# Performance work log

Hardware: AMD Instinct MI355X
Metric: run time of the kernel (lower is better)

The kernel has to match this reference:

```python
import jax, jax.numpy as jnp
import numpy as np

WL_W = 8   # wl_weight
WL_IN = 8  # wl_activate (input quantization)
EPS = 1e-5

def _wq(x, bits):
    # WAGE-style uniform quantize-dequantize to `bits` bits in [-1+step, 1-step], STE passthrough
    step = 2.0 ** (1 - bits)
    q = jnp.clip(jnp.round(x / step) * step, -1.0 + step, 1.0 - step)
    return x + jax.lax.stop_gradient(q - x)

def _qconv(x, w, b, pad):
    y = jax.lax.conv_general_dilated(
        _wq(x, WL_IN), _wq(w, WL_W), (1, 1), [(pad, pad), (pad, pad)],
        dimension_numbers=('NCHW', 'OIHW', 'NCHW'))
    return y + b[None, :, None, None]

def _bn_relu(x, g, be):
    # BatchNorm2d in training mode: batch statistics over (N, H, W)
    m = jnp.mean(x, axis=(0, 2, 3), keepdims=True)
    v = jnp.var(x, axis=(0, 2, 3), keepdims=True)
    return jax.nn.relu((x - m) * jax.lax.rsqrt(v + EPS) * g[None, :, None, None] + be[None, :, None, None])

def _maxpool3(x):
    # MaxPool2d(3, stride=1, padding=1)
    return jax.lax.reduce_window(x, -jnp.inf, jax.lax.max,
                                 (1, 1, 3, 3), (1, 1, 1, 1),
                                 [(0, 0), (0, 0), (1, 1), (1, 1)])

def setup_inputs() -> dict:
    key = jax.random.key(0)
    ks = jax.random.split(key, 8)
    d = {'x': jax.random.normal(ks[0], (128, 192, 32, 32), jnp.float32)}
    specs = [('b1', 1, 64, 192, 1), ('b2a', 2, 96, 192, 1), ('b2b', 3, 128, 96, 3),
             ('b3a', 4, 16, 192, 1), ('b3b', 5, 32, 16, 3), ('b3c', 6, 32, 32, 3),
             ('b4', 7, 32, 192, 1)]
    for name, i, co, ci, k in specs:
        d[name + '_w'] = jax.random.normal(ks[i], (co, ci, k, k), jnp.float32) * 0.05
        d[name + '_b'] = jnp.zeros((co,), jnp.float32)
        d[name + '_g'] = jnp.ones((co,), jnp.float32)
        d[name + '_be'] = jnp.zeros((co,), jnp.float32)
    return d

def reference(x,
              b1_w, b1_b, b1_g, b1_be,
              b2a_w, b2a_b, b2a_g, b2a_be,
              b2b_w, b2b_b, b2b_g, b2b_be,
              b3a_w, b3a_b, b3a_g, b3a_be,
              b3b_w, b3b_b, b3b_g, b3b_be,
              b3c_w, b3c_b, b3c_g, b3c_be,
              b4_w, b4_b, b4_g, b4_be):
    y1 = _bn_relu(_qconv(x, b1_w, b1_b, 0), b1_g, b1_be)
    y2 = _bn_relu(_qconv(x, b2a_w, b2a_b, 0), b2a_g, b2a_be)
    y2 = _bn_relu(_qconv(y2, b2b_w, b2b_b, 1), b2b_g, b2b_be)
    y3 = _bn_relu(_qconv(x, b3a_w, b3a_b, 0), b3a_g, b3a_be)
    y3 = _bn_relu(_qconv(y3, b3b_w, b3b_b, 1), b3b_g, b3b_be)
    y3 = _bn_relu(_qconv(y3, b3c_w, b3c_b, 1), b3c_g, b3c_be)
    y4 = _bn_relu(_qconv(_maxpool3(x), b4_w, b4_b, 0), b4_g, b4_be)
    return jnp.concatenate([y1, y2, y3, y4], axis=1)  # [N, 256, 32, 32]
```

## Files before the change

### kernel.cpp

```cpp
#include <hip/hip_runtime.h>

typedef unsigned short u16;
typedef unsigned int u32;
typedef __attribute__((ext_vector_type(4))) int i32x4;
typedef __attribute__((ext_vector_type(4))) float f32x4;
typedef __attribute__((ext_vector_type(4))) u16 u16x4;
typedef __attribute__((ext_vector_type(8))) u16 u16x8;

#define PTOT 131072
#define NREP 16

static __device__ __forceinline__ int qi8(float v) {
  int q = (int)rintf(v * 128.f);
  return max(-127, min(127, q));
}
static __device__ __forceinline__ u16 bf_rne(float v) {
  u32 u = __float_as_uint(v);
  u += 0x7fffu + ((u >> 16) & 1u);
  return (u16)(u >> 16);
}
static __device__ __forceinline__ float bf2f(u16 v) {
  return __uint_as_float((u32)v << 16);
}

struct WPtrs { const float* p[7]; };

__global__ void wpack_kernel(WPtrs wp, char* __restrict__ o) {
  static const int S[7][5] = {
      {0,      192, 192, 1, 64},
      {12288,  192, 192, 1, 96},
      {30720,  96,  320, 3, 128},
      {153600, 192, 192, 1, 16},
      {156672, 16,  64,  3, 32},
      {162816, 32,  128, 3, 32},
      {175104, 192, 192, 1, 32},
  };
  int idx = blockIdx.x * 256 + threadIdx.x;
  if (idx >= 181248) return;
  int s = 0;
#pragma unroll
  for (int i = 1; i < 7; ++i)
    if (idx >= S[i][0]) s = i;
  int local = idx - S[s][0];
  int CIr = S[s][1], KROWP = S[s][2], KH = S[s][3], Co = S[s][4];
  int j = local & 15, lane = (local >> 4) & 63, f = local >> 10;
  int NF = Co >> 4;
  int c = f / NF, nf = f - c * NF;
  int co = nf * 16 + (lane & 15);
  int k = c * 64 + ((lane >> 4) << 4) + j;
  int r = k / KROWP, kk = k - r * KROWP;
  char val = 0;
  if (kk < 3 * CIr || KH == 1) {
    int kw = (KH == 1) ? 0 : (kk / CIr);
    int ci = (KH == 1) ? kk : (kk - kw * CIr);
    val = (char)qi8(wp.p[s][(((size_t)co * CIr + ci) * KH + r) * KH + kw]);
  }
  o[idx] = val;
}

__global__ __launch_bounds__(256) void quantx_kernel(const float* __restrict__ x,
                                                     char* __restrict__ xq) {
  __shared__ __align__(16) char tile[64][80];
  int n = blockIdx.z, hwb = blockIdx.x * 64, cb = blockIdx.y * 64;
  int lane = threadIdx.x & 63, sub = threadIdx.x >> 6;
#pragma unroll
  for (int i = 0; i < 16; ++i) {
    int c = sub + i * 4;
    float v = x[(((size_t)n * 192 + cb + c) << 10) + hwb + lane];
    tile[lane][c] = (char)qi8(v);
  }
  __syncthreads();
  int t = threadIdx.x, px = t >> 2, c16 = t & 3;
  uint4 v = *(const uint4*)&tile[px][c16 * 16];
  *(uint4*)&xq[(((size_t)n << 10) + hwb + px) * 192 + cb + c16 * 16] = v;
}

__global__ __launch_bounds__(256) void pool_kernel(const char* __restrict__ xq,
                                                   char* __restrict__ xpq) {
  int idx = blockIdx.x * 256 + threadIdx.x;
  int c16 = idx % 12;
  int p = idx / 12;
  int n = p >> 10, hw = p & 1023, h = hw >> 5, w = hw & 31;
  int m[16];
#pragma unroll
  for (int j = 0; j < 16; ++j) m[j] = -127;
  for (int dh = -1; dh <= 1; ++dh) {
    int hh = h + dh; if (hh < 0 || hh > 31) continue;
    for (int dw = -1; dw <= 1; ++dw) {
      int ww = w + dw; if (ww < 0 || ww > 31) continue;
      uint4 v = *(const uint4*)&xq[((((size_t)n << 5) + hh) * 32 + ww) * 192 + c16 * 16];
      const char* bb = reinterpret_cast<const char*>(&v);
#pragma unroll
      for (int t = 0; t < 16; ++t) {
        int b = (int)bb[t];
        m[t] = b > m[t] ? b : m[t];
      }
    }
  }
  uint4 o;
  char* ob = reinterpret_cast<char*>(&o);
#pragma unroll
  for (int t = 0; t < 16; ++t) ob[t] = (char)m[t];
  *(uint4*)&xpq[(size_t)p * 192 + c16 * 16] = o;
}

__global__ __launch_bounds__(256) void border_kernel(char* __restrict__ q2a,
                                                     char* __restrict__ q3a,
                                                     char* __restrict__ q3b) {
  int img = blockIdx.x, buf = blockIdx.y;
  char* base; int C;
  if (buf == 0) { base = q2a; C = 96; }
  else if (buf == 1) { base = q3a; C = 16; }
  else { base = q3b; C = 32; }
  char* ib = base + (size_t)img * 34 * 34 * C;
  int nch = C >> 4;
  uint4 z = {0, 0, 0, 0};
  for (int idx = threadIdx.x; idx < 132 * nch; idx += 256) {
    int b = idx / nch, cc = idx - b * nch;
    int h, w;
    if (b < 34) { h = 0; w = b; }
    else if (b < 68) { h = 33; w = b - 34; }
    else { int s = b - 68; h = 1 + (s >> 1); w = (s & 1) ? 33 : 0; }
    *(uint4*)(ib + ((h * 34 + w) * C + cc * 16)) = z;
  }
}

template <int NFW, int MF>
static __device__ __forceinline__ void conv_epilogue(
    i32x4 (&acc)[MF][NFW], int nfw, int lane, int wave, int mbase,
    u16* __restrict__ yh, double* __restrict__ stb, int ststride) {
  float yv[MF][NFW][4];
#pragma unroll
  for (int mf = 0; mf < MF; ++mf)
#pragma unroll
    for (int nf = 0; nf < NFW; ++nf)
      if (nf < nfw) {
        int col = nf * 16 + (lane & 15);
        int pix = mbase + mf * 16 + ((lane >> 4) << 2);
        u16x4 o;
#pragma unroll
        for (int r = 0; r < 4; ++r) {
          float v = (float)acc[mf][nf][r] * 6.103515625e-05f;
          yv[mf][nf][r] = v;
          o[r] = bf_rne(v);
        }
        *(u16x4*)&yh[(size_t)col * PTOT + pix] = o;
      }

  float s1[NFW], s2[NFW];
#pragma unroll
  for (int nf = 0; nf < NFW; ++nf) { s1[nf] = 0.f; s2[nf] = 0.f; }
#pragma unroll
  for (int mf = 0; mf < MF; ++mf)
#pragma unroll
    for (int nf = 0; nf < NFW; ++nf)
      if (nf < nfw)
#pragma unroll
        for (int r = 0; r < 4; ++r) {
          float v = yv[mf][nf][r];
          s1[nf] += v;
          s2[nf] += v * v;
        }
#pragma unroll
  for (int m = 16; m <= 32; m <<= 1)
#pragma unroll
    for (int nf = 0; nf < NFW; ++nf) {
      s1[nf] += __shfl_xor(s1[nf], m);
      s2[nf] += __shfl_xor(s2[nf], m);
    }
  __shared__ float red[4][NFW][16][2];
  if (lane < 16)
#pragma unroll
    for (int nf = 0; nf < NFW; ++nf) {
      red[wave][nf][lane][0] = s1[nf];
      red[wave][nf][lane][1] = s2[nf];
    }
  __syncthreads();
  const int t = threadIdx.x;
  if (t < 16 * nfw) {
    int nf = t >> 4, l = t & 15;
    float a = red[0][nf][l][0] + red[1][nf][l][0] + red[2][nf][l][0] + red[3][nf][l][0];
    float b = red[0][nf][l][1] + red[1][nf][l][1] + red[2][nf][l][1] + red[3][nf][l][1];
    int rep = blockIdx.x & (NREP - 1);
    atomicAdd(&stb[rep * ststride + 2 * t], (double)a);
    atomicAdd(&stb[rep * ststride + 2 * t + 1], (double)b);
  }
}

__global__ __launch_bounds__(256, 4) void cstat1x1_kernel(
    const char* __restrict__ xq, const char* __restrict__ xpq,
    const char* __restrict__ bpk, double* __restrict__ st, u16* __restrict__ yh) {
  constexpr int NFW = 6;
  constexpr int MF = 2;
  const int b = blockIdx.y;
  const int nfw = (b == 0) ? 4 : (b == 1) ? 6 : (b == 2) ? 1 : 2;
  const int bpo = (b == 0) ? 0 : (b == 1) ? 12288 : (b == 2) ? 153600 : 175104;
  const int sto = (b == 0) ? 0 : (b == 1) ? 256 * NREP
                           : (b == 2) ? 3 * 256 * NREP : 6 * 256 * NREP;
  const int yho = (b == 0) ? 0 : (b == 1) ? 64 : (b == 2) ? 160 : 176;
  const char* xin = (b == 3) ? xpq : xq;
  const char* bp = bpk + bpo;
  double* stb = st + sto;
  u16* yhb = yh + (size_t)yho * PTOT;

  const int lane = threadIdx.x & 63;
  const int wave = threadIdx.x >> 6;
  const int mbase = blockIdx.x * 128 + wave * 32;

  uint abase[MF];
#pragma unroll
  for (int mf = 0; mf < MF; ++mf)
    abase[mf] = (uint)(mbase + mf * 16 + (lane & 15)) * 192u;
  const uint klane = (uint)(lane >> 4) * 16u;
  const uint blane = (uint)lane * 16u;

  i32x4 acc[MF][NFW];
#pragma unroll
  for (int i = 0; i < MF; ++i)
#pragma unroll
    for (int j = 0; j < NFW; ++j) acc[i][j] = {0, 0, 0, 0};

#pragma unroll
  for (int c = 0; c < 3; ++c) {
    i32x4 af[MF];
#pragma unroll
    for (int mf = 0; mf < MF; ++mf)
      af[mf] = *(const i32x4*)(xin + (abase[mf] + (uint)c * 64u + klane));
    i32x4 bfr[NFW];
#pragma unroll
    for (int nf = 0; nf < NFW; ++nf)
      if (nf < nfw)
        bfr[nf] = *(const i32x4*)(bp + ((uint)((c * nfw + nf) * 1024) + blane));
#pragma unroll
    for (int mf = 0; mf < MF; ++mf)
#pragma unroll
      for (int nf = 0; nf < NFW; ++nf)
        if (nf < nfw)
          acc[mf][nf] = __builtin_amdgcn_mfma_i32_16x16x64_i8(af[mf], bfr[nf],
                                                              acc[mf][nf], 0, 0, 0);
  }

  conv_epilogue<NFW, MF>(acc, nfw, lane, wave, mbase, yhb, stb, 256);
}

template <int CI, int KROWP, int COB, int WPEU>
__global__ __launch_bounds__(256, WPEU) void cstat9_kernel(
    const char* __restrict__ xin, const char* __restrict__ bp, int nft,
    double* __restrict__ stb, u16* __restrict__ yh) {
  constexpr int CPR = KROWP / 64;
  constexpr int NCH = 3 * CPR;
  constexpr int NFW = COB / 16;
  constexpr int MF = 2;
  constexpr int TILE = 6 * 34 * CI;
  constexpr int TV = TILE / 16;

  __shared__ __align__(16) char atile[TILE + 64];

  const int lane = threadIdx.x & 63;
  const int wave = threadIdx.x >> 6;
  const int mbase = blockIdx.x * 128 + wave * 32;

  {
    int p0 = blockIdx.x * 128;
    int n = p0 >> 10, h0 = (p0 & 1023) >> 5;
    const char* src = xin + (size_t)((n * 34 + h0) * 34) * CI;
    for (int s = threadIdx.x; s < TV; s += 256)
      *(uint4*)&atile[s * 16] = *(const uint4*)(src + (size_t)s * 16);
  }
  __syncthreads();

  uint albase[MF];
#pragma unroll
  for (int mf = 0; mf < MF; ++mf) {
    int lp = wave * 32 + mf * 16 + (lane & 15);
    albase[mf] = (uint)(((lp >> 5) * 34 + (lp & 31)) * CI);
  }
  const uint klane = (uint)(lane >> 4) * 16u;
  const uint blane = (uint)lane * 16u;

  i32x4 acc[MF][NFW];
#pragma unroll
  for (int i = 0; i < MF; ++i)
#pragma unroll
    for (int j = 0; j < NFW; ++j) acc[i][j] = {0, 0, 0, 0};

#pragma unroll 2
  for (int c = 0; c < NCH; ++c) {
    int rr = c / CPR, o = (c - rr * CPR) * 64;
    uint koff = (uint)(rr * 34 * CI + o);
    i32x4 af[MF];
#pragma unroll
    for (int mf = 0; mf < MF; ++mf)
      af[mf] = *(const i32x4*)&atile[albase[mf] + koff + klane];
    i32x4 bfr[NFW];
#pragma unroll
    for (int nf = 0; nf < NFW; ++nf)
      bfr[nf] = *(const i32x4*)(bp + ((uint)((c * nft + nf) * 1024) + blane));
#pragma unroll
    for (int mf = 0; mf < MF; ++mf)
#pragma unroll
      for (int nf = 0; nf < NFW; ++nf)
        acc[mf][nf] = __builtin_amdgcn_mfma_i32_16x16x64_i8(af[mf], bfr[nf],
                                                            acc[mf][nf], 0, 0, 0);
  }

  conv_epilogue<NFW, MF>(acc, NFW, lane, wave, mbase, yh, stb, 256);
}

struct BnPtrs { const float* g[4]; const float* be[4]; };

__global__ __launch_bounds__(256) void bnout_all_kernel(
    const u16* __restrict__ yh, const double* __restrict__ st, BnPtrs bp,
    float* __restrict__ out) {
  int co = blockIdx.y, chunk = blockIdx.x, tid = threadIdx.x;
  int br = (co < 64) ? 0 : (co < 192) ? 1 : (co < 224) ? 2 : 3;
  int lco = co - ((br == 0) ? 0 : (br == 1) ? 64 : (br == 2) ? 192 : 224);
  int yhoff = (br == 0) ? 0 : (br == 1) ? 208 : (br == 2) ? 368 : 176;
  int stoff = (br == 0) ? 0 : (br == 1) ? 2 * 256 * NREP
                         : (br == 2) ? 5 * 256 * NREP : 6 * 256 * NREP;
  const double* stb = st + stoff;
  double s1d = 0., s2d = 0.;
#pragma unroll
  for (int r = 0; r < NREP; ++r) {
    s1d += stb[r * 256 + 2 * lco];
    s2d += stb[r * 256 + 2 * lco + 1];
  }
  double m = s1d * (1.0 / PTOT);
  double v = s2d * (1.0 / PTOT) - m * m;
  double inv = 1.0 / sqrt(v + 1e-5);
  double c0d = (double)bp.g[br][lco] * inv;
  float c0 = (float)c0d;
  float c1 = (float)((double)bp.be[br][lco] - m * c0d);

  int p0 = chunk * 4096 + tid * 16;
  int n = p0 >> 10, hw = p0 & 1023;
  const u16* yp = yh + (size_t)(yhoff + lco) * PTOT + p0;
  float* op = out + (((size_t)(n * 256 + co)) << 10) + hw;
#pragma unroll
  for (int half = 0; half < 2; ++half) {
    u16x8 r = *(const u16x8*)(yp + half * 8);
    f32x4 a, b;
#pragma unroll
    for (int e = 0; e < 4; ++e) {
      a[e] = fmaxf(fmaf(bf2f(r[e]), c0, c1), 0.f);
      b[e] = fmaxf(fmaf(bf2f(r[e + 4]), c0, c1), 0.f);
    }
    *(f32x4*)(op + half * 8) = a;
    *(f32x4*)(op + half * 8 + 4) = b;
  }
}

template <int CO, int COP>
__global__ __launch_bounds__(256) void bnqpad_kernel(const u16* __restrict__ yh,
                                                     const double* __restrict__ stb,
                                                     const float* __restrict__ g,
                                                     const float* __restrict__ be,
                                                     char* __restrict__ q) {
  __shared__ float2 cfl[CO];
  __shared__ __align__(16) char tile[64][COP + 16];
  const int t = threadIdx.x;
  if (t < CO) {
    double s1d = 0., s2d = 0.;
#pragma unroll
    for (int r = 0; r < NREP; ++r) {
      s1d += stb[r * 256 + 2 * t];
      s2d += stb[r * 256 + 2 * t + 1];
    }
    double m = s1d * (1.0 / PTOT);
    double v = s2d * (1.0 / PTOT) - m * m;
    double inv = 1.0 / sqrt(v + 1e-5);
    double c0 = (double)g[t] * inv;
    cfl[t] = make_float2((float)c0, (float)((double)be[t] - m * c0));
  }
  __syncthreads();
  int p0 = blockIdx.x * 64;
  int lane = t & 63, sub = t >> 6;
#pragma unroll
  for (int i = 0; i < COP / 4; ++i) {
    int co = sub + i * 4;
    float2 cc = cfl[co];
    float z = fmaxf(fmaf(bf2f(yh[(size_t)co * PTOT + p0 + lane]), cc.x, cc.y), 0.f);
    tile[lane][co] = (char)min((int)rintf(z * 128.f), 127);
  }
  __syncthreads();
  for (int chunk = t; chunk < 64 * (COP / 16); chunk += 256) {
    int px = chunk / (COP / 16), c16 = chunk % (COP / 16);
    int p = p0 + px;
    int n = p >> 10, hw = p & 1023, h = hw >> 5, w = hw & 31;
    size_t dst = (((size_t)n * 34 + h + 1) * 34 + (w + 1)) * COP + c16 * 16;
    *(uint4*)&q[dst] = *(const uint4*)&tile[px][c16 * 16];
  }
}

extern "C" void kernel_launch(void* const* d_in, const int* in_sizes, int n_in,
                              void* d_out, int out_size, void* d_ws, size_t ws_size,
                              hipStream_t stream) {
  const float* x = (const float*)d_in[0];
  float* out = (float*)d_out;
  char* ws = (char*)d_ws;

  if (ws_size < 155599872ull) return;
  char* xq  = ws;
  char* xpq = ws + 25165824ull;
  char* q2a = xpq;
  char* q3a = ws + 39371008ull;
  char* q3b = ws + 41738752ull;
  u16* yh   = (u16*)(ws + 50331648ull);
  char* bpk = ws + 155189248ull;
  double* st = (double*)(ws + 155370496ull);

  hipMemsetAsync(st, 0, 7 * NREP * 256 * 8, stream);

  WPtrs wp;
  const int widx[7] = {1, 5, 9, 13, 17, 21, 25};
  for (int i = 0; i < 7; ++i) wp.p[i] = (const float*)d_in[widx[i]];
  wpack_kernel<<<708, 256, 0, stream>>>(wp, bpk);

  quantx_kernel<<<dim3(16, 3, 128), 256, 0, stream>>>(x, xq);
  pool_kernel<<<6144, 256, 0, stream>>>(xq, xpq);

  double* stB[7];
  for (int b = 0; b < 7; ++b) stB[b] = st + (size_t)b * NREP * 256;

  cstat1x1_kernel<<<dim3(1024, 4), 256, 0, stream>>>(xq, xpq, bpk, st, yh);

  border_kernel<<<dim3(128, 3), 256, 0, stream>>>(q2a, q3a, q3b);

  bnqpad_kernel<96, 96><<<2048, 256, 0, stream>>>(yh + (size_t)64 * PTOT, stB[1],
                                                  (const float*)d_in[7],
                                                  (const float*)d_in[8], q2a);
  cstat9_kernel<96, 320, 128, 3><<<1024, 256, 0, stream>>>(
      q2a, bpk + 30720, 8, stB[2], yh + (size_t)208 * PTOT);

  bnqpad_kernel<16, 16><<<2048, 256, 0, stream>>>(yh + (size_t)160 * PTOT, stB[3],
                                                  (const float*)d_in[15],
                                                  (const float*)d_in[16], q3a);
  cstat9_kernel<16, 64, 32, 4><<<1024, 256, 0, stream>>>(
      q3a, bpk + 156672, 2, stB[4], yh + (size_t)336 * PTOT);
  bnqpad_kernel<32, 32><<<2048, 256, 0, stream>>>(yh + (size_t)336 * PTOT, stB[4],
                                                  (const float*)d_in[19],
                                                  (const float*)d_in[20], q3b);
  cstat9_kernel<32, 128, 32, 4><<<1024, 256, 0, stream>>>(
      q3b, bpk + 162816, 2, stB[5], yh + (size_t)368 * PTOT);

  BnPtrs bp;
  bp.g[0] = (const float*)d_in[3];  bp.be[0] = (const float*)d_in[4];
  bp.g[1] = (const float*)d_in[11]; bp.be[1] = (const float*)d_in[12];
  bp.g[2] = (const float*)d_in[23]; bp.be[2] = (const float*)d_in[24];
  bp.g[3] = (const float*)d_in[27]; bp.be[3] = (const float*)d_in[28];
  bnout_all_kernel<<<dim3(32, 256), 256, 0, stream>>>(yh, st, bp, out);
}
```

Before: 215.6 us.

## Fuse BN-ReLU-quantize-pad into 3x3 conv tile loads, drop border and bnqpad kernels

Each 3x3 conv now reads the previous stage's bf16 pre-BN output directly. It computes the BN coefficients per block, applies BN+ReLU+int8 quantization while filling the shared tile, and zeroes the tile for padding. This removes the separate bnqpad and border kernels, their launches, and the padded int8 intermediate buffers. In exchange each block recomputes the BN coefficients and requantizes halo rows, about 6/4 redundant reads. The byte-wise scattered LDS writes may also cause bank conflicts.

```diff
diff --git a/kernel.cpp b/kernel.cpp
--- a/kernel.cpp
+++ b/kernel.cpp
@@ -104,27 +104,6 @@
   *(uint4*)&xpq[(size_t)p * 192 + c16 * 16] = o;
 }
 
-__global__ __launch_bounds__(256) void border_kernel(char* __restrict__ q2a,
-                                                     char* __restrict__ q3a,
-                                                     char* __restrict__ q3b) {
-  int img = blockIdx.x, buf = blockIdx.y;
-  char* base; int C;
-  if (buf == 0) { base = q2a; C = 96; }
-  else if (buf == 1) { base = q3a; C = 16; }
-  else { base = q3b; C = 32; }
-  char* ib = base + (size_t)img * 34 * 34 * C;
-  int nch = C >> 4;
-  uint4 z = {0, 0, 0, 0};
-  for (int idx = threadIdx.x; idx < 132 * nch; idx += 256) {
-    int b = idx / nch, cc = idx - b * nch;
-    int h, w;
-    if (b < 34) { h = 0; w = b; }
-    else if (b < 68) { h = 33; w = b - 34; }
-    else { int s = b - 68; h = 1 + (s >> 1); w = (s & 1) ? 33 : 0; }
-    *(uint4*)(ib + ((h * 34 + w) * C + cc * 16)) = z;
-  }
-}
-
 template <int NFW, int MF>
 static __device__ __forceinline__ void conv_epilogue(
     i32x4 (&acc)[MF][NFW], int nfw, int lane, int wave, int mbase,
@@ -244,36 +223,71 @@
 }
 
 template <int CI, int KROWP, int COB, int WPEU>
-__global__ __launch_bounds__(256, WPEU) void cstat9_kernel(
-    const char* __restrict__ xin, const char* __restrict__ bp, int nft,
+__global__ __launch_bounds__(256, WPEU) void cstat9q_kernel(
+    const u16* __restrict__ yhin, const double* __restrict__ stp,
+    const float* __restrict__ gp, const float* __restrict__ bep,
+    const char* __restrict__ bp, int nft,
     double* __restrict__ stb, u16* __restrict__ yh) {
   constexpr int CPR = KROWP / 64;
   constexpr int NCH = 3 * CPR;
   constexpr int NFW = COB / 16;
   constexpr int MF = 2;
   constexpr int TILE = 6 * 34 * CI;
-  constexpr int TV = TILE / 16;
 
   __shared__ __align__(16) char atile[TILE + 64];
-
-  const int lane = threadIdx.x & 63;
-  const int wave = threadIdx.x >> 6;
+  __shared__ float2 cfl[CI];
+
+  const int tid = threadIdx.x;
+
+  if (tid < CI) {
+    double s1d = 0., s2d = 0.;
+#pragma unroll
+    for (int r = 0; r < NREP; ++r) {
+      s1d += stp[r * 256 + 2 * tid];
+      s2d += stp[r * 256 + 2 * tid + 1];
+    }
+    double m = s1d * (1.0 / PTOT);
+    double v = s2d * (1.0 / PTOT) - m * m;
+    double inv = 1.0 / sqrt(v + 1e-5);
+    double c0 = (double)gp[tid] * inv;
+    cfl[tid] = make_float2((float)c0, (float)((double)bep[tid] - m * c0));
+  }
+  {
+    uint4 z = {0, 0, 0, 0};
+    for (int s = tid * 16; s < TILE + 64; s += 4096) *(uint4*)&atile[s] = z;
+  }
+  __syncthreads();
+
+  const int p0 = blockIdx.x * 128;
+  const int n = p0 >> 10, h0 = (p0 & 1023) >> 5;
+  for (int task = tid; task < CI * 6; task += 256) {
+    int co = task / 6, rr = task - co * 6;
+    int irow = h0 - 1 + rr;
+    if (irow < 0 || irow > 31) continue;
+    const u16* src = yhin + (size_t)co * PTOT + (n << 10) + (irow << 5);
+    float2 cc = cfl[co];
+    char* dst = &atile[(rr * 34 + 1) * CI + co];
+#pragma unroll
+    for (int w8 = 0; w8 < 4; ++w8) {
+      u16x8 v = *(const u16x8*)(src + w8 * 8);
+#pragma unroll
+      for (int e = 0; e < 8; ++e) {
+        float z = fmaxf(fmaf(bf2f(v[e]), cc.x, cc.y), 0.f);
+        dst[(w8 * 8 + e) * CI] = (char)min((int)rintf(z * 128.f), 127);
+      }
+    }
+  }
+  __syncthreads();
+
+  const int lane = tid & 63;
+  const int wave = tid >> 6;
   const int mbase = blockIdx.x * 128 + wave * 32;
-
-  {
-    int p0 = blockIdx.x * 128;
-    int n = p0 >> 10, h0 = (p0 & 1023) >> 5;
-    const char* src = xin + (size_t)((n * 34 + h0) * 34) * CI;
-    for (int s = threadIdx.x; s < TV; s += 256)
-      *(uint4*)&atile[s * 16] = *(const uint4*)(src + (size_t)s * 16);
-  }
-  __syncthreads();
 
   uint albase[MF];
 #pragma unroll
   for (int mf = 0; mf < MF; ++mf) {
     int lp = wave * 32 + mf * 16 + (lane & 15);
-    albase[mf] = (uint)(((lp >> 5) * 34 + (lp & 31)) * CI);
+    albase[mf] = (uint)((((lp >> 5) + 1) * 34 + 1 + (lp & 31)) * CI);
   }
   const uint klane = (uint)(lane >> 4) * 16u;
   const uint blane = (uint)lane * 16u;
@@ -287,7 +301,7 @@
 #pragma unroll 2
   for (int c = 0; c < NCH; ++c) {
     int rr = c / CPR, o = (c - rr * CPR) * 64;
-    uint koff = (uint)(rr * 34 * CI + o);
+    uint koff = (uint)((rr - 1) * 34 * CI + o - CI);
     i32x4 af[MF];
 #pragma unroll
     for (int mf = 0; mf < MF; ++mf)
@@ -350,48 +364,6 @@
   }
 }
 
-template <int CO, int COP>
-__global__ __launch_bounds__(256) void bnqpad_kernel(const u16* __restrict__ yh,
-                                                     const double* __restrict__ stb,
-                                                     const float* __restrict__ g,
-                                                     const float* __restrict__ be,
-                                                     char* __restrict__ q) {
-  __shared__ float2 cfl[CO];
-  __shared__ __align__(16) char tile[64][COP + 16];
-  const int t = threadIdx.x;
-  if (t < CO) {
-    double s1d = 0., s2d = 0.;
-#pragma unroll
-    for (int r = 0; r < NREP; ++r) {
-      s1d += stb[r * 256 + 2 * t];
-      s2d += stb[r * 256 + 2 * t + 1];
-    }
-    double m = s1d * (1.0 / PTOT);
-    double v = s2d * (1.0 / PTOT) - m * m;
-    double inv = 1.0 / sqrt(v + 1e-5);
-    double c0 = (double)g[t] * inv;
-    cfl[t] = make_float2((float)c0, (float)((double)be[t] - m * c0));
-  }
-  __syncthreads();
-  int p0 = blockIdx.x * 64;
-  int lane = t & 63, sub = t >> 6;
-#pragma unroll
-  for (int i = 0; i < COP / 4; ++i) {
-    int co = sub + i * 4;
-    float2 cc = cfl[co];
-    float z = fmaxf(fmaf(bf2f(yh[(size_t)co * PTOT + p0 + lane]), cc.x, cc.y), 0.f);
-    tile[lane][co] = (char)min((int)rintf(z * 128.f), 127);
-  }
-  __syncthreads();
-  for (int chunk = t; chunk < 64 * (COP / 16); chunk += 256) {
-    int px = chunk / (COP / 16), c16 = chunk % (COP / 16);
-    int p = p0 + px;
-    int n = p >> 10, hw = p & 1023, h = hw >> 5, w = hw & 31;
-    size_t dst = (((size_t)n * 34 + h + 1) * 34 + (w + 1)) * COP + c16 * 16;
-    *(uint4*)&q[dst] = *(const uint4*)&tile[px][c16 * 16];
-  }
-}
-
 extern "C" void kernel_launch(void* const* d_in, const int* in_sizes, int n_in,
                               void* d_out, int out_size, void* d_ws, size_t ws_size,
                               hipStream_t stream) {
@@ -402,9 +374,6 @@
   if (ws_size < 155599872ull) return;
   char* xq  = ws;
   char* xpq = ws + 25165824ull;
-  char* q2a = xpq;
-  char* q3a = ws + 39371008ull;
-  char* q3b = ws + 41738752ull;
   u16* yh   = (u16*)(ws + 50331648ull);
   char* bpk = ws + 155189248ull;
   double* st = (double*)(ws + 155370496ull);
@@ -424,24 +393,17 @@
 
   cstat1x1_kernel<<<dim3(1024, 4), 256, 0, stream>>>(xq, xpq, bpk, st, yh);
 
-  border_kernel<<<dim3(128, 3), 256, 0, stream>>>(q2a, q3a, q3b);
-
-  bnqpad_kernel<96, 96><<<2048, 256, 0, stream>>>(yh + (size_t)64 * PTOT, stB[1],
-                                                  (const float*)d_in[7],
-                                                  (const float*)d_in[8], q2a);
-  cstat9_kernel<96, 320, 128, 3><<<1024, 256, 0, stream>>>(
-      q2a, bpk + 30720, 8, stB[2], yh + (size_t)208 * PTOT);
-
-  bnqpad_kernel<16, 16><<<2048, 256, 0, stream>>>(yh + (size_t)160 * PTOT, stB[3],
-                                                  (const float*)d_in[15],
-                                                  (const float*)d_in[16], q3a);
-  cstat9_kernel<16, 64, 32, 4><<<1024, 256, 0, stream>>>(
-      q3a, bpk + 156672, 2, stB[4], yh + (size_t)336 * PTOT);
-  bnqpad_kernel<32, 32><<<2048, 256, 0, stream>>>(yh + (size_t)336 * PTOT, stB[4],
-                                                  (const float*)d_in[19],
-                                                  (const float*)d_in[20], q3b);
-  cstat9_kernel<32, 128, 32, 4><<<1024, 256, 0, stream>>>(
-      q3b, bpk + 162816, 2, stB[5], yh + (size_t)368 * PTOT);
+  cstat9q_kernel<96, 320, 128, 3><<<1024, 256, 0, stream>>>(
+      yh + (size_t)64 * PTOT, stB[1], (const float*)d_in[7], (const float*)d_in[8],
+      bpk + 30720, 8, stB[2], yh + (size_t)208 * PTOT);
+
+  cstat9q_kernel<16, 64, 32, 4><<<1024, 256, 0, stream>>>(
+      yh + (size_t)160 * PTOT, stB[3], (const float*)d_in[15], (const float*)d_in[16],
+      bpk + 156672, 2, stB[4], yh + (size_t)336 * PTOT);
+
+  cstat9q_kernel<32, 128, 32, 4><<<1024, 256, 0, stream>>>(
+      yh + (size_t)336 * PTOT, stB[4], (const float*)d_in[19], (const float*)d_in[20],
+      bpk + 162816, 2, stB[5], yh + (size_t)368 * PTOT);
 
   BnPtrs bp;
   bp.g[0] = (const float*)d_in[3];  bp.be[0] = (const float*)d_in[4];
```

Result: faster. 206.9 us (-4.0%).
